# Performance work log

Hardware: AMD Instinct MI355X
Metric: run time of the kernel (lower is better)

## Reference

```python
import jax, jax.numpy as jnp
import numpy as np

B, S, D, H = 2, 2048, 1024, 16
DK = D // H


def setup_inputs() -> dict:
    key = jax.random.key(0)
    ks = jax.random.split(key, 9)
    sc = 0.02
    return {
        "x": jax.random.normal(ks[0], (B, S, D), dtype=jnp.float32),
        "attention_mask": jnp.ones((B, S), dtype=jnp.int32),
        "Wq": jax.random.normal(ks[1], (D, D), dtype=jnp.float32) * sc,
        "bq": jax.random.normal(ks[2], (D,), dtype=jnp.float32) * sc,
        "Wk": jax.random.normal(ks[3], (D, D), dtype=jnp.float32) * sc,
        "bk": jax.random.normal(ks[4], (D,), dtype=jnp.float32) * sc,
        "Wv": jax.random.normal(ks[5], (D, D), dtype=jnp.float32) * sc,
        "bv": jax.random.normal(ks[6], (D,), dtype=jnp.float32) * sc,
        "Wo": jax.random.normal(ks[7], (D, D), dtype=jnp.float32) * sc,
        "bo": jax.random.normal(ks[8], (D,), dtype=jnp.float32) * sc,
    }


def reference(x, attention_mask, Wq, bq, Wk, bk, Wv, bv, Wo, bo):
    b, s, d = x.shape
    # projections (Linear: x @ W + b) then split heads -> [b, h, s, dk]
    def heads(t):
        return t.reshape(b, s, H, DK).transpose(0, 2, 1, 3)
    Q = heads(x @ Wq + bq)
    K = heads(x @ Wk + bk)
    V = heads(x @ Wv + bv)
    # NOTE: original computes K @ Q^T (not Q @ K^T) and applies NO 1/sqrt(dk) scale
    scores = jnp.einsum("bhid,bhjd->bhij", K, Q)  # [b, h, s, s]
    causal = jnp.tril(jnp.ones((s, s), dtype=bool))  # [s, s]
    final_mask = attention_mask[:, None, None, :].astype(bool) & causal[None, None]
    scores = jnp.where(final_mask, scores, -jnp.inf)
    attn = jax.nn.softmax(scores, axis=-1)
    out = jnp.einsum("bhij,bhjd->bhid", attn, V)  # [b, h, s, dk]
    out = out.transpose(0, 2, 1, 3).reshape(b, s, d)
    return out @ Wo + bo
```

## Files before the change

kernel.cpp:

```cpp
#include <hip/hip_runtime.h>
#include <stdint.h>
#include <stddef.h>


typedef short bf16x8 __attribute__((ext_vector_type(8)));
typedef float f32x4  __attribute__((ext_vector_type(4)));

__device__ __forceinline__ short f2bf(float f) {
  union { float f; uint32_t u; } a; a.f = f;
  uint32_t r = a.u + 0x7fffu + ((a.u >> 16) & 1u);
  return (short)(r >> 16);
}
__device__ __forceinline__ float bf2f(short s) {
  union { uint32_t u; float f; } a; a.u = ((uint32_t)(uint16_t)s) << 16;
  return a.f;
}
__device__ __forceinline__ uint32_t pack2bf(float a, float b) {
  union { float f; uint32_t u; } x, y; x.f = a; y.f = b;
  return (x.u >> 16) | (y.u & 0xffff0000u);
}
__device__ __forceinline__ float fast_exp2(float x) {
#if __has_builtin(__builtin_amdgcn_exp2f)
  return __builtin_amdgcn_exp2f(x);
#else
  return exp2f(x);
#endif
}
__device__ __forceinline__ void async16(const void* g, void* l) {
  __builtin_amdgcn_global_load_lds(
      (const __attribute__((address_space(1))) uint32_t*)g,
      (__attribute__((address_space(3))) uint32_t*)l, 16, 0, 0);
}
#define MFMA(a, b, c) __builtin_amdgcn_mfma_f32_16x16x32_bf16((a), (b), (c), 0, 0, 0)

__global__ void k_split_x(const float* __restrict__ x, short* __restrict__ xhi) {
  int i = blockIdx.x * 256 + threadIdx.x;
  float4 v = ((const float4*)x)[i];
  short4 h;
  h.x = f2bf(v.x);
  h.y = f2bf(v.y);
  h.z = f2bf(v.z);
  h.w = f2bf(v.w);
  ((short4*)xhi)[i] = h;
}

__global__ void k_prep_w(const float* __restrict__ Wq, const float* __restrict__ Wk,
                         const float* __restrict__ Wv, const float* __restrict__ Wo,
                         short* __restrict__ whi, short* __restrict__ wo) {
  __shared__ float T[64][65];
  int z = blockIdx.z;
  const float* W = (z == 0) ? Wq : (z == 1) ? Wk : (z == 2) ? Wv : Wo;
  int n0 = blockIdx.x * 64, k0 = blockIdx.y * 64;
  int t = threadIdx.x;
  int rr = t >> 4, cc = (t & 15) * 4;
#pragma unroll
  for (int it = 0; it < 4; ++it) {
    int row = rr + it * 16;
    float4 v = *(const float4*)&W[(size_t)(k0 + row) * 1024 + n0 + cc];
    T[row][cc] = v.x; T[row][cc + 1] = v.y; T[row][cc + 2] = v.z; T[row][cc + 3] = v.w;
  }
  __syncthreads();
  short* oh = (z < 3) ? (whi + (size_t)z * 1048576) : wo;
#pragma unroll
  for (int it = 0; it < 4; ++it) {
    int nrow = rr + it * 16;
    short4 h4;
    h4.x = f2bf(T[cc + 0][nrow]);
    h4.y = f2bf(T[cc + 1][nrow]);
    h4.z = f2bf(T[cc + 2][nrow]);
    h4.w = f2bf(T[cc + 3][nrow]);
    *(short4*)&oh[(size_t)(n0 + nrow) * 1024 + k0 + cc] = h4;
  }
}

__global__ __launch_bounds__(256, 3) void k_gemm_qkv(
    const short* __restrict__ xhi, const short* __restrict__ whi,
    const float* __restrict__ bq, const float* __restrict__ bk,
    const float* __restrict__ bv,
    short* __restrict__ Qhi, short* __restrict__ Qlo,
    short* __restrict__ Khi, short* __restrict__ Klo,
    short* __restrict__ Vt) {
  __shared__ short AH[2][4096];
  __shared__ short BH[2][4096];
  int tid = threadIdx.x;
  int bx = blockIdx.x;
  int m0 = blockIdx.y * 128;
  int n0g = bx * 128;
  int w = tid >> 6, lane = tid & 63, lr = lane & 15, lq = lane >> 4;
  int wm = w >> 1, wn = w & 1;
  f32x4 acc[4][4] = {};

  auto stage = [&](int ks, int pb) {
#pragma unroll
    for (int it = 0; it < 2; ++it) {
      int idx = it * 256 + tid;
      int row = idx >> 2, c = idx & 3;
      int cs = c ^ (row & 3);
      async16(xhi + (size_t)(m0 + row) * 1024 + ks * 32 + cs * 8, &AH[pb][idx * 8]);
      async16(whi + (size_t)(n0g + row) * 1024 + ks * 32 + cs * 8, &BH[pb][idx * 8]);
    }
  };

  stage(0, 0);
  int p = 0;
  int g = lq ^ (lr & 3);
  for (int ks = 0; ks < 32; ++ks) {
    __syncthreads();
    if (ks < 31) stage(ks + 1, p ^ 1);
    const bf16x8* A8 = (const bf16x8*)AH[p];
    const bf16x8* B8 = (const bf16x8*)BH[p];
    bf16x8 af[4], bfr[4];
#pragma unroll
    for (int mt = 0; mt < 4; ++mt) af[mt] = A8[(wm * 64 + mt * 16 + lr) * 4 + g];
#pragma unroll
    for (int nt = 0; nt < 4; ++nt) bfr[nt] = B8[(wn * 64 + nt * 16 + lr) * 4 + g];
#pragma unroll
    for (int mt = 0; mt < 4; ++mt)
#pragma unroll
      for (int nt = 0; nt < 4; ++nt)
        acc[mt][nt] = MFMA(af[mt], bfr[nt], acc[mt][nt]);
    p ^= 1;
  }

  int z = bx >> 3;
  const float LOG2E = 1.44269504f;
  if (z == 2) {
#pragma unroll
    for (int nt = 0; nt < 4; ++nt) {
      int dg = (n0g & 1023) + wn * 64 + nt * 16 + lr;
      float bvv = bv[dg];
      int hh = dg >> 6, dk = dg & 63;
#pragma unroll
      for (int mt = 0; mt < 4; ++mt) {
        int row = m0 + wm * 64 + mt * 16 + lq * 4;
        int b_ = row >> 11, s_ = row & 2047;
        short4 pk;
        pk.x = f2bf(acc[mt][nt][0] + bvv);
        pk.y = f2bf(acc[mt][nt][1] + bvv);
        pk.z = f2bf(acc[mt][nt][2] + bvv);
        pk.w = f2bf(acc[mt][nt][3] + bvv);
        *(short4*)&Vt[(size_t)((b_ * 16 + hh) * 64 + dk) * 2048 + s_] = pk;
      }
    }
  } else {
    const float* bias = (z == 0) ? bq : bk;
    short* Ch = (z == 0) ? Qhi : Khi;
    short* Cl = (z == 0) ? Qlo : Klo;
#pragma unroll
    for (int nt = 0; nt < 4; ++nt) {
      int colg = (n0g & 1023) + wn * 64 + nt * 16 + lr;
      float bvv = bias[colg];
#pragma unroll
      for (int mt = 0; mt < 4; ++mt)
#pragma unroll
        for (int r = 0; r < 4; ++r) {
          int row = m0 + wm * 64 + mt * 16 + lq * 4 + r;
          float v = acc[mt][nt][r] + bvv;
          if (z == 0) v *= LOG2E;
          size_t o = (size_t)row * 1024 + colg;
          short hh = f2bf(v);
          Ch[o] = hh;
          Cl[o] = f2bf(v - bf2f(hh));
        }
    }
  }
}

__global__ __launch_bounds__(256, 3) void k_gemm_o(
    const short* __restrict__ Ab, const short* __restrict__ Bb,
    const float* __restrict__ bias, float* __restrict__ Cf) {
  __shared__ short AH[2][4096];
  __shared__ short BH[2][4096];
  int tid = threadIdx.x;
  int m0 = blockIdx.y * 128, n0 = blockIdx.x * 128;
  int w = tid >> 6, lane = tid & 63, lr = lane & 15, lq = lane >> 4;
  int wm = w >> 1, wn = w & 1;
  f32x4 acc[4][4] = {};

  auto stage = [&](int ks, int pb) {
#pragma unroll
    for (int it = 0; it < 2; ++it) {
      int idx = it * 256 + tid;
      int row = idx >> 2, c = idx & 3;
      int cs = c ^ (row & 3);
      async16(Ab + (size_t)(m0 + row) * 1024 + ks * 32 + cs * 8, &AH[pb][idx * 8]);
      async16(Bb + (size_t)(n0 + row) * 1024 + ks * 32 + cs * 8, &BH[pb][idx * 8]);
    }
  };

  stage(0, 0);
  int p = 0;
  int g = lq ^ (lr & 3);
  for (int ks = 0; ks < 32; ++ks) {
    __syncthreads();
    if (ks < 31) stage(ks + 1, p ^ 1);
    const bf16x8* A8 = (const bf16x8*)AH[p];
    const bf16x8* B8 = (const bf16x8*)BH[p];
    bf16x8 af[4], bfr[4];
#pragma unroll
    for (int mt = 0; mt < 4; ++mt) af[mt] = A8[(wm * 64 + mt * 16 + lr) * 4 + g];
#pragma unroll
    for (int nt = 0; nt < 4; ++nt) bfr[nt] = B8[(wn * 64 + nt * 16 + lr) * 4 + g];
#pragma unroll
    for (int mt = 0; mt < 4; ++mt)
#pragma unroll
      for (int nt = 0; nt < 4; ++nt)
        acc[mt][nt] = MFMA(af[mt], bfr[nt], acc[mt][nt]);
    p ^= 1;
  }

#pragma unroll
  for (int nt = 0; nt < 4; ++nt) {
    int col = n0 + wn * 64 + nt * 16 + lr;
    float bvv = bias[col];
#pragma unroll
    for (int mt = 0; mt < 4; ++mt)
#pragma unroll
      for (int r = 0; r < 4; ++r) {
        int row = m0 + wm * 64 + mt * 16 + lq * 4 + r;
        Cf[(size_t)row * 1024 + col] = acc[mt][nt][r] + bvv;
      }
  }
}

__global__ __launch_bounds__(256, 3) void k_attn(
    const short* __restrict__ Khi, const short* __restrict__ Klo,
    const short* __restrict__ Qhi, const short* __restrict__ Qlo,
    const short* __restrict__ Vt, const int* __restrict__ amask,
    short* __restrict__ Obuf) {
  __shared__ short QH[2][4096];
  __shared__ short QL[2][4096];
  __shared__ short VS[2][4096];
  int tid = threadIdx.x;
  int bid = blockIdx.x;
  int xcd = bid & 7, idx = bid >> 3;
  int bh = xcd * 4 + (idx & 3);
  int L  = 32 - (idx >> 2);
  int b = bh >> 4, h = bh & 15;
  int w = tid >> 6, lane = tid & 63, lr = lane & 15, lq = lane >> 4;
  int band = 2 * (L - 1) + (w >> 1);
  int rb0 = band * 32 + (w & 1) * 16;

  bf16x8 kh[2], kl[2];
  {
    size_t ra = ((size_t)(b * 2048 + rb0 + lr)) * 1024 + h * 64;
#pragma unroll
    for (int ks = 0; ks < 2; ++ks) {
      kh[ks] = *(const bf16x8*)(Khi + ra + ks * 32 + lq * 8);
      kl[ks] = *(const bf16x8*)(Klo + ra + ks * 32 + lq * 8);
    }
  }

  f32x4 O[4] = {};
  float ls = 0.f;
  int iq = rb0 + lr;
  int baddr0 = (((lq & 1) * 2) * 16 + lr) * 4;
  int baddr1 = baddr0 + 64;

  auto stage = [&](int jt, int pb) {
    int j0 = jt * 64;
#pragma unroll
    for (int it = 0; it < 2; ++it) {
      int idx2 = it * 256 + tid;
      int rr = idx2 >> 3, c = idx2 & 7;
      int cs = c ^ (rr & 7);
      size_t gq = ((size_t)(b * 2048 + j0 + rr)) * 1024 + h * 64 + cs * 8;
      async16(Qhi + gq, &QH[pb][idx2 * 8]);
      async16(Qlo + gq, &QL[pb][idx2 * 8]);
      size_t gv = ((size_t)(bh * 64 + rr)) * 2048 + j0 + cs * 8;
      async16(Vt + gv, &VS[pb][idx2 * 8]);
    }
  };

  stage(0, 0);
  int p = 0;
  for (int t = 0; t < L; ++t) {
    __syncthreads();
    if (t + 1 < L) stage(t + 1, p ^ 1);
    int j0 = t * 64;
    const bf16x8* Q8 = (const bf16x8*)QH[p];
    const bf16x8* L8 = (const bf16x8*)QL[p];
    const bf16x8* V8 = (const bf16x8*)VS[p];

    int av = amask[b * 2048 + j0 + lane];
    unsigned long long bal = __ballot(av != 0);
    bool allv = (bal == ~0ull);

    f32x4 s[4] = {};
#pragma unroll
    for (int mt = 0; mt < 4; ++mt) {
      int row = mt * 16 + lr;
#pragma unroll
      for (int ks = 0; ks < 2; ++ks) {
        int gi = row * 8 + ((ks * 4 + lq) ^ (row & 7));
        bf16x8 qa = Q8[gi];
        bf16x8 la = L8[gi];
        s[mt] = MFMA(qa, kh[ks], s[mt]);
        s[mt] = MFMA(la, kh[ks], s[mt]);
        s[mt] = MFMA(qa, kl[ks], s[mt]);
      }
    }

    bool diag = (t == L - 1);
    float pv[4][4];
#pragma unroll
    for (int mt = 0; mt < 4; ++mt)
#pragma unroll
      for (int r = 0; r < 4; ++r)
        pv[mt][r] = fast_exp2(s[mt][r]);
    if (diag) {
#pragma unroll
      for (int mt = 0; mt < 4; ++mt)
#pragma unroll
        for (int r = 0; r < 4; ++r)
          if (j0 + mt * 16 + lq * 4 + r > iq) pv[mt][r] = 0.f;
    }
    if (!allv) {
#pragma unroll
      for (int mt = 0; mt < 4; ++mt)
#pragma unroll
        for (int r = 0; r < 4; ++r)
          if (!((bal >> (mt * 16 + lq * 4 + r)) & 1)) pv[mt][r] = 0.f;
    }
    uint32_t pd[4][2];
#pragma unroll
    for (int mt = 0; mt < 4; ++mt) {
      ls += (pv[mt][0] + pv[mt][1]) + (pv[mt][2] + pv[mt][3]);
      pd[mt][0] = pack2bf(pv[mt][0], pv[mt][1]);
      pd[mt][1] = pack2bf(pv[mt][2], pv[mt][3]);
    }

#pragma unroll
    for (int k2 = 0; k2 < 2; ++k2) {
      union { int i[4]; bf16x8 v; } pa;
#pragma unroll
      for (int dd = 0; dd < 4; ++dd) {
        int addr = (dd >> 1) ? baddr1 : baddr0;
        int v0 = __builtin_amdgcn_ds_bpermute(addr, (int)pd[k2 * 2 + 0][dd & 1]);
        int v1 = __builtin_amdgcn_ds_bpermute(addr, (int)pd[k2 * 2 + 1][dd & 1]);
        pa.i[dd] = (lq >> 1) ? v1 : v0;
      }
#pragma unroll
      for (int nt = 0; nt < 4; ++nt) {
        int row = nt * 16 + lr;
        bf16x8 vb = V8[row * 8 + ((k2 * 4 + lq) ^ (row & 7))];
        O[nt] = MFMA(pa.v, vb, O[nt]);
      }
    }
    p ^= 1;
  }

  float tsum = ls;
  tsum += __shfl_xor(tsum, 16);
  tsum += __shfl_xor(tsum, 32);
  float inv[4];
#pragma unroll
  for (int r = 0; r < 4; ++r) inv[r] = 1.0f / __shfl(tsum, lq * 4 + r, 64);
#pragma unroll
  for (int nt = 0; nt < 4; ++nt)
#pragma unroll
    for (int r = 0; r < 4; ++r) {
      int row = b * 2048 + rb0 + lq * 4 + r;
      int col = h * 64 + nt * 16 + lr;
      Obuf[(size_t)row * 1024 + col] = f2bf(O[nt][r] * inv[r]);
    }
}

extern "C" void kernel_launch(void* const* d_in, const int* in_sizes, int n_in,
                              void* d_out, int out_size, void* d_ws, size_t ws_size,
                              hipStream_t stream) {
  const float* x  = (const float*)d_in[0];
  const int* amask = (const int*)d_in[1];
  const float* Wq = (const float*)d_in[2];
  const float* bq = (const float*)d_in[3];
  const float* Wk = (const float*)d_in[4];
  const float* bk = (const float*)d_in[5];
  const float* Wv = (const float*)d_in[6];
  const float* bv = (const float*)d_in[7];
  const float* Wo = (const float*)d_in[8];
  const float* bo = (const float*)d_in[9];

  char* ws = (char*)d_ws;
  const size_t MB = 1024 * 1024;
  short* xhi = (short*)(ws);
  short* whi = (short*)(ws + 16 * MB);
  short* wo  = (short*)(ws + 26 * MB);
  short* Qhi = (short*)(ws + 28 * MB);
  short* Qlo = (short*)(ws + 36 * MB);
  short* Khi = (short*)(ws + 44 * MB);
  short* Klo = (short*)(ws + 52 * MB);
  short* Vt  = (short*)(ws + 60 * MB);
  short* Obuf = xhi;

  k_split_x<<<4096, 256, 0, stream>>>(x, xhi);
  k_prep_w<<<dim3(16, 16, 4), 256, 0, stream>>>(Wq, Wk, Wv, Wo, whi, wo);

  k_gemm_qkv<<<dim3(24, 32), 256, 0, stream>>>(xhi, whi, bq, bk, bv,
                                               Qhi, Qlo, Khi, Klo, Vt);
  k_attn<<<1024, 256, 0, stream>>>(Khi, Klo, Qhi, Qlo, Vt, amask, Obuf);
  k_gemm_o<<<dim3(8, 32), 256, 0, stream>>>(Obuf, wo, bo, (float*)d_out);
}
```

Measured before the change: 209.4 us.

## Split KV tiles across wave pairs, each wave computing 32 query rows

Each wave pair now shares a 32-row band. Each wave holds K fragments for both 16-row groups and processes only alternating key tiles (even or odd t), instead of every wave processing all tiles for 16 rows. The partial O accumulators and row sums are combined through LDS scratch at the end. This reuses each LDS Q/V fragment read across two row groups, halving LDS traffic per MFMA and raising independent MFMA chains. In exchange it doubles accumulator registers, which may hurt occupancy at launch bounds (256,3), and it adds an LDS reduction step.

```diff
diff --git a/kernel.cpp b/kernel.cpp
--- a/kernel.cpp
+++ b/kernel.cpp
@@ -238,22 +238,23 @@
   int L  = 32 - (idx >> 2);
   int b = bh >> 4, h = bh & 15;
   int w = tid >> 6, lane = tid & 63, lr = lane & 15, lq = lane >> 4;
-  int band = 2 * (L - 1) + (w >> 1);
-  int rb0 = band * 32 + (w & 1) * 16;
-
-  bf16x8 kh[2], kl[2];
-  {
-    size_t ra = ((size_t)(b * 2048 + rb0 + lr)) * 1024 + h * 64;
+  int wc = w >> 1;
+  int wq = w & 1;
+  int band = 2 * (L - 1) + wc;
+
+  bf16x8 kh[2][2], kl[2][2];
+#pragma unroll
+  for (int ig = 0; ig < 2; ++ig) {
+    size_t ra = ((size_t)(b * 2048 + band * 32 + ig * 16 + lr)) * 1024 + h * 64;
 #pragma unroll
     for (int ks = 0; ks < 2; ++ks) {
-      kh[ks] = *(const bf16x8*)(Khi + ra + ks * 32 + lq * 8);
-      kl[ks] = *(const bf16x8*)(Klo + ra + ks * 32 + lq * 8);
-    }
-  }
-
-  f32x4 O[4] = {};
-  float ls = 0.f;
-  int iq = rb0 + lr;
+      kh[ig][ks] = *(const bf16x8*)(Khi + ra + ks * 32 + lq * 8);
+      kl[ig][ks] = *(const bf16x8*)(Klo + ra + ks * 32 + lq * 8);
+    }
+  }
+
+  f32x4 O0[4] = {}, O1[4] = {};
+  float ls0 = 0.f, ls1 = 0.f;
   int baddr0 = (((lq & 1) * 2) * 16 + lr) * 4;
   int baddr1 = baddr0 + 64;
 
@@ -273,20 +274,20 @@
   };
 
   stage(0, 0);
-  int p = 0;
   for (int t = 0; t < L; ++t) {
     __syncthreads();
-    if (t + 1 < L) stage(t + 1, p ^ 1);
+    if (t + 1 < L) stage(t + 1, (t + 1) & 1);
+    if ((t & 1) != wq) continue;
     int j0 = t * 64;
-    const bf16x8* Q8 = (const bf16x8*)QH[p];
-    const bf16x8* L8 = (const bf16x8*)QL[p];
-    const bf16x8* V8 = (const bf16x8*)VS[p];
+    const bf16x8* Q8 = (const bf16x8*)QH[t & 1];
+    const bf16x8* L8 = (const bf16x8*)QL[t & 1];
+    const bf16x8* V8 = (const bf16x8*)VS[t & 1];
 
     int av = amask[b * 2048 + j0 + lane];
     unsigned long long bal = __ballot(av != 0);
     bool allv = (bal == ~0ull);
 
-    f32x4 s[4] = {};
+    f32x4 s0[4] = {}, s1[4] = {};
 #pragma unroll
     for (int mt = 0; mt < 4; ++mt) {
       int row = mt * 16 + lr;
@@ -295,75 +296,107 @@
         int gi = row * 8 + ((ks * 4 + lq) ^ (row & 7));
         bf16x8 qa = Q8[gi];
         bf16x8 la = L8[gi];
-        s[mt] = MFMA(qa, kh[ks], s[mt]);
-        s[mt] = MFMA(la, kh[ks], s[mt]);
-        s[mt] = MFMA(qa, kl[ks], s[mt]);
+        s0[mt] = MFMA(qa, kh[0][ks], s0[mt]);
+        s1[mt] = MFMA(qa, kh[1][ks], s1[mt]);
+        s0[mt] = MFMA(la, kh[0][ks], s0[mt]);
+        s1[mt] = MFMA(la, kh[1][ks], s1[mt]);
+        s0[mt] = MFMA(qa, kl[0][ks], s0[mt]);
+        s1[mt] = MFMA(qa, kl[1][ks], s1[mt]);
       }
     }
 
     bool diag = (t == L - 1);
-    float pv[4][4];
-#pragma unroll
-    for (int mt = 0; mt < 4; ++mt)
-#pragma unroll
-      for (int r = 0; r < 4; ++r)
-        pv[mt][r] = fast_exp2(s[mt][r]);
-    if (diag) {
-#pragma unroll
-      for (int mt = 0; mt < 4; ++mt)
-#pragma unroll
-        for (int r = 0; r < 4; ++r)
-          if (j0 + mt * 16 + lq * 4 + r > iq) pv[mt][r] = 0.f;
-    }
-    if (!allv) {
-#pragma unroll
-      for (int mt = 0; mt < 4; ++mt)
-#pragma unroll
-        for (int r = 0; r < 4; ++r)
-          if (!((bal >> (mt * 16 + lq * 4 + r)) & 1)) pv[mt][r] = 0.f;
-    }
-    uint32_t pd[4][2];
-#pragma unroll
-    for (int mt = 0; mt < 4; ++mt) {
-      ls += (pv[mt][0] + pv[mt][1]) + (pv[mt][2] + pv[mt][3]);
-      pd[mt][0] = pack2bf(pv[mt][0], pv[mt][1]);
-      pd[mt][1] = pack2bf(pv[mt][2], pv[mt][3]);
+    uint32_t pd[2][4][2];
+#pragma unroll
+    for (int ig = 0; ig < 2; ++ig) {
+      int iqg = band * 32 + ig * 16 + lr;
+      float lsl = 0.f;
+#pragma unroll
+      for (int mt = 0; mt < 4; ++mt) {
+        f32x4 sv = ig ? s1[mt] : s0[mt];
+        float pv[4];
+#pragma unroll
+        for (int r = 0; r < 4; ++r) pv[r] = fast_exp2(sv[r]);
+        if (diag) {
+#pragma unroll
+          for (int r = 0; r < 4; ++r)
+            if (j0 + mt * 16 + lq * 4 + r > iqg) pv[r] = 0.f;
+        }
+        if (!allv) {
+#pragma unroll
+          for (int r = 0; r < 4; ++r)
+            if (!((bal >> (mt * 16 + lq * 4 + r)) & 1)) pv[r] = 0.f;
+        }
+        lsl += (pv[0] + pv[1]) + (pv[2] + pv[3]);
+        pd[ig][mt][0] = pack2bf(pv[0], pv[1]);
+        pd[ig][mt][1] = pack2bf(pv[2], pv[3]);
+      }
+      if (ig) ls1 += lsl; else ls0 += lsl;
     }
 
 #pragma unroll
     for (int k2 = 0; k2 < 2; ++k2) {
-      union { int i[4]; bf16x8 v; } pa;
+      union { int i[4]; bf16x8 v; } pa0, pa1;
 #pragma unroll
       for (int dd = 0; dd < 4; ++dd) {
         int addr = (dd >> 1) ? baddr1 : baddr0;
-        int v0 = __builtin_amdgcn_ds_bpermute(addr, (int)pd[k2 * 2 + 0][dd & 1]);
-        int v1 = __builtin_amdgcn_ds_bpermute(addr, (int)pd[k2 * 2 + 1][dd & 1]);
-        pa.i[dd] = (lq >> 1) ? v1 : v0;
+        int a0 = __builtin_amdgcn_ds_bpermute(addr, (int)pd[0][k2 * 2 + 0][dd & 1]);
+        int a1 = __builtin_amdgcn_ds_bpermute(addr, (int)pd[0][k2 * 2 + 1][dd & 1]);
+        pa0.i[dd] = (lq >> 1) ? a1 : a0;
+        int b0 = __builtin_amdgcn_ds_bpermute(addr, (int)pd[1][k2 * 2 + 0][dd & 1]);
+        int b1 = __builtin_amdgcn_ds_bpermute(addr, (int)pd[1][k2 * 2 + 1][dd & 1]);
+        pa1.i[dd] = (lq >> 1) ? b1 : b0;
       }
 #pragma unroll
       for (int nt = 0; nt < 4; ++nt) {
         int row = nt * 16 + lr;
         bf16x8 vb = V8[row * 8 + ((k2 * 4 + lq) ^ (row & 7))];
-        O[nt] = MFMA(pa.v, vb, O[nt]);
-      }
-    }
-    p ^= 1;
-  }
-
-  float tsum = ls;
-  tsum += __shfl_xor(tsum, 16);
-  tsum += __shfl_xor(tsum, 32);
-  float inv[4];
-#pragma unroll
-  for (int r = 0; r < 4; ++r) inv[r] = 1.0f / __shfl(tsum, lq * 4 + r, 64);
-#pragma unroll
-  for (int nt = 0; nt < 4; ++nt)
+        O0[nt] = MFMA(pa0.v, vb, O0[nt]);
+        O1[nt] = MFMA(pa1.v, vb, O1[nt]);
+      }
+    }
+  }
+
+  __syncthreads();
+  float* scr = (wc == 0) ? (float*)&QH[0][0] : (float*)&QL[0][0];
+  float ts0 = ls0; ts0 += __shfl_xor(ts0, 16); ts0 += __shfl_xor(ts0, 32);
+  float ts1 = ls1; ts1 += __shfl_xor(ts1, 16); ts1 += __shfl_xor(ts1, 32);
+  if (wq == 0) {
+#pragma unroll
+    for (int nt = 0; nt < 4; ++nt)
+#pragma unroll
+      for (int r = 0; r < 4; ++r) {
+        scr[(lq * 4 + r) * 68 + nt * 16 + lr] = O0[nt][r];
+        scr[(16 + lq * 4 + r) * 68 + nt * 16 + lr] = O1[nt][r];
+      }
+    if (lq == 0) {
+      scr[lr * 68 + 64] = ts0;
+      scr[(16 + lr) * 68 + 64] = ts1;
+    }
+  }
+  __syncthreads();
+  if (wq == 1) {
+    ts0 += scr[lr * 68 + 64];
+    ts1 += scr[(16 + lr) * 68 + 64];
+    float inv0[4], inv1[4];
 #pragma unroll
     for (int r = 0; r < 4; ++r) {
-      int row = b * 2048 + rb0 + lq * 4 + r;
-      int col = h * 64 + nt * 16 + lr;
-      Obuf[(size_t)row * 1024 + col] = f2bf(O[nt][r] * inv[r]);
-    }
+      inv0[r] = 1.0f / __shfl(ts0, lq * 4 + r, 64);
+      inv1[r] = 1.0f / __shfl(ts1, lq * 4 + r, 64);
+    }
+#pragma unroll
+    for (int nt = 0; nt < 4; ++nt)
+#pragma unroll
+      for (int r = 0; r < 4; ++r) {
+        int col = h * 64 + nt * 16 + lr;
+        float o0 = O0[nt][r] + scr[(lq * 4 + r) * 68 + nt * 16 + lr];
+        int row0 = b * 2048 + band * 32 + lq * 4 + r;
+        Obuf[(size_t)row0 * 1024 + col] = f2bf(o0 * inv0[r]);
+        float o1 = O1[nt][r] + scr[(16 + lq * 4 + r) * 68 + nt * 16 + lr];
+        int row1 = row0 + 16;
+        Obuf[(size_t)row1 * 1024 + col] = f2bf(o1 * inv1[r]);
+      }
+  }
 }
 
 extern "C" void kernel_launch(void* const* d_in, const int* in_sizes, int n_in,
```

Result: slower. 245.4 us (+17.2%).
